# Performance work log

Hardware: AMD Instinct MI355X
Metric: run time of the kernel (lower is better)

Reference implementation:

```python
import jax, jax.numpy as jnp
import numpy as np

N_HEAD = 32
N_KV_HEAD = 8
HD = 64  # head dim
N_EMBD = 2048
B, T = 2, 2048
ROPE_THETA = 10000.0


def _apply_rope(x, cos, sin):
    # x: [B, T, H, HD]; cos/sin: [T, HD//2]. Interleaved complex pairs (even, odd),
    # matching torch.view_as_complex on x.reshape(..., -1, 2).
    x0 = x[..., 0::2]
    x1 = x[..., 1::2]
    c = cos[None, :, None, :]
    s = sin[None, :, None, :]
    o0 = x0 * c - x1 * s
    o1 = x0 * s + x1 * c
    return jnp.stack([o0, o1], axis=-1).reshape(x.shape)


def setup_inputs() -> dict:
    key = jax.random.key(0)
    k1, k2, k3 = jax.random.split(key, 3)
    x = jax.random.normal(k1, (B, T, N_EMBD), dtype=jnp.float32)
    Wqkv = jax.random.normal(k2, ((N_HEAD + 2 * N_KV_HEAD) * HD, N_EMBD), dtype=jnp.float32) * 0.02
    Wproj = jax.random.normal(k3, (N_EMBD, N_EMBD), dtype=jnp.float32) * 0.02
    # precompute_freqs_cis as in llm.c (llama path)
    freqs = 1.0 / (ROPE_THETA ** (np.arange(0, HD, 2, dtype=np.float32) / HD))
    ang = np.outer(np.arange(T, dtype=np.float32), freqs)  # [T, HD//2]
    freqs_cos = jnp.asarray(np.cos(ang), dtype=jnp.float32)
    freqs_sin = jnp.asarray(np.sin(ang), dtype=jnp.float32)
    return {"x": x, "Wqkv": Wqkv, "Wproj": Wproj,
            "freqs_cos": freqs_cos, "freqs_sin": freqs_sin, "start_pos": -1}


def reference(x, Wqkv, Wproj, freqs_cos, freqs_sin, start_pos):
    Bx, Tx, C = x.shape
    n_rep = N_HEAD // N_KV_HEAD
    qkv = x @ Wqkv.T  # [B, T, (H + 2*KV)*HD]
    q = qkv[..., : N_HEAD * HD].reshape(Bx, Tx, N_HEAD, HD)
    k = qkv[..., N_HEAD * HD: (N_HEAD + N_KV_HEAD) * HD].reshape(Bx, Tx, N_KV_HEAD, HD)
    v = qkv[..., (N_HEAD + N_KV_HEAD) * HD:].reshape(Bx, Tx, N_KV_HEAD, HD)
    # RoPE on q, k
    q = _apply_rope(q, freqs_cos, freqs_sin)
    k = _apply_rope(k, freqs_cos, freqs_sin)
    # start_pos < 0: training path, no KV cache. GQA repeat of kv heads.
    k = jnp.repeat(k, n_rep, axis=2)  # [B, T, H, HD]
    v = jnp.repeat(v, n_rep, axis=2)
    q = q.transpose(0, 2, 1, 3)  # [B, H, T, HD]
    k = k.transpose(0, 2, 1, 3)
    v = v.transpose(0, 2, 1, 3)
    scale = 1.0 / np.sqrt(HD).astype(np.float32)
    scores = jnp.einsum("bhtd,bhsd->bhts", q, k) * scale  # [B, H, T, T]
    causal = jnp.tril(jnp.ones((Tx, Tx), dtype=bool))
    scores = jnp.where(causal[None, None, :, :], scores, -jnp.inf)
    att = jax.nn.softmax(scores.astype(jnp.float32), axis=-1).astype(q.dtype)
    y = jnp.einsum("bhts,bhsd->bhtd", att, v)
    y = y.transpose(0, 2, 1, 3).reshape(Bx, Tx, C)
    return y @ Wproj.T
```

## Files before the change

### kernel.cpp

```cpp
#include <hip/hip_runtime.h>
#include <hip/hip_bf16.h>
#include <cstdint>

#define NH   32
#define NKV  8
#define HD   64
#define CE   2048
#define BB   2
#define TT   2048
#define QKVD 3072
#define MM   (BB*TT)

typedef float  f32x4  __attribute__((ext_vector_type(4)));
typedef float  f32x16 __attribute__((ext_vector_type(16)));
typedef short  s16x8  __attribute__((ext_vector_type(8)));
typedef unsigned short u16;

#define AS1 __attribute__((address_space(1)))
#define AS3 __attribute__((address_space(3)))
#define GLDS16(src, dst) __builtin_amdgcn_global_load_lds( \
    (const AS1 uint32_t*)(src), (AS3 uint32_t*)(dst), 16, 0, 0)

static __device__ __forceinline__ float bf2f(u16 u) {
    union { uint32_t u; float f; } v; v.u = ((uint32_t)u) << 16; return v.f;
}
static __device__ __forceinline__ u16 f2bf(float f) {
    union { float f; uint32_t u; } v; v.f = f;
    uint32_t r = v.u + 0x7fffu + ((v.u >> 16) & 1u);
    return (u16)(r >> 16);
}
static __device__ __forceinline__ uint32_t cvtpk(float lo, float hi) {
    uint32_t r;
    asm("v_cvt_pk_bf16_f32 %0, %1, %2" : "=v"(r) : "v"(lo), "v"(hi));
    return r;
}
static __device__ __forceinline__ void plswap(uint32_t &a, uint32_t &b) {
    asm volatile("v_permlane32_swap_b32 %0, %1" : "+v"(a), "+v"(b));
}

static __device__ __forceinline__ void cvt8(const float* __restrict__ in, uint32_t* __restrict__ out) {
    const float4* p = reinterpret_cast<const float4*>(in);
    float4 a = p[0], b = p[1];
    uint4 o;
    o.x = cvtpk(a.x, a.y); o.y = cvtpk(a.z, a.w);
    o.z = cvtpk(b.x, b.y); o.w = cvtpk(b.z, b.w);
    *reinterpret_cast<uint4*>(out) = o;
}
__global__ void k_cvt_all(const float* __restrict__ x, const float* __restrict__ wqkv,
                          const float* __restrict__ wproj,
                          uint32_t* __restrict__ xo, uint32_t* __restrict__ wqo,
                          uint32_t* __restrict__ wpo,
                          const float* __restrict__ fcos, const float* __restrict__ fsin,
                          float2* __restrict__ csT) {
    const int n1 = MM * CE / 8, n2 = QKVD * CE / 8, n3 = CE * CE / 8, n4 = 32 * TT / 8;
    int i = blockIdx.x * blockDim.x + threadIdx.x;
    if (i < n1) {
        cvt8(x + (size_t)i * 8, xo + (size_t)i * 4);
    } else if (i < n1 + n2) {
        int k = i - n1;
        cvt8(wqkv + (size_t)k * 8, wqo + (size_t)k * 4);
    } else if (i < n1 + n2 + n3) {
        int k = i - n1 - n2;
        cvt8(wproj + (size_t)k * 8, wpo + (size_t)k * 4);
    } else if (i < n1 + n2 + n3 + n4) {
        int k = (i - n1 - n2 - n3) * 8;
        #pragma unroll
        for (int jj = 0; jj < 8; ++jj) {
            float2 cs; cs.x = fcos[k + jj]; cs.y = fsin[k + jj];
            csT[k + jj] = cs;
        }
    }
}

__global__ __launch_bounds__(256) void k_gemm_qkv(const u16* __restrict__ A,
                                                  const u16* __restrict__ Bm,
                                                  u16* __restrict__ Qb,
                                                  u16* __restrict__ Kb,
                                                  u16* __restrict__ Vt,
                                                  const float2* __restrict__ csT) {
    __shared__ u16 As[128 * 32];
    __shared__ u16 Bs[128 * 32];
    const int K = CE;
    const int c  = blockIdx.x + 24 * blockIdx.y;
    const int nc = (c & 7) * 96 + (c >> 3);
    const int m0 = (nc / 24) * 128;
    const int n0 = (nc % 24) * 128;

    const int tid  = threadIdx.x;
    const int w    = tid >> 6;
    const int lane = tid & 63;
    const int lr   = lane & 15, lg = lane >> 4;
    const int wm   = (w >> 1) * 64, wn = (w & 1) * 64;

    const int o0 = w * 2048 + lane * 16, o1 = o0 + 1024;
    const int ar0 = o0 >> 6, ar1 = o1 >> 6;
    const int ac0 = (o0 & 63) >> 1, ac1 = (o1 & 63) >> 1;
    const size_t aof0 = (size_t)(m0 + ar0) * K + ac0;
    const size_t aof1 = (size_t)(m0 + ar1) * K + ac1;
    const size_t bof0 = (size_t)(n0 + ar0) * K + ac0;
    const size_t bof1 = (size_t)(n0 + ar1) * K + ac1;
    u16* dA0 = &As[w * 1024];       u16* dA1 = &As[w * 1024 + 512];
    u16* dB0 = &Bs[w * 1024];       u16* dB1 = &Bs[w * 1024 + 512];

    f32x4 acc[4][4] = {};

    for (int k0 = 0; k0 < K; k0 += 32) {
        GLDS16(A  + aof0 + k0, dA0);
        GLDS16(A  + aof1 + k0, dA1);
        GLDS16(Bm + bof0 + k0, dB0);
        GLDS16(Bm + bof1 + k0, dB1);
        __syncthreads();
        s16x8 af[4], bf[4];
        #pragma unroll
        for (int i = 0; i < 4; ++i)
            af[i] = *reinterpret_cast<const s16x8*>(&As[(wm + i * 16 + lr) * 32 + lg * 8]);
        #pragma unroll
        for (int j = 0; j < 4; ++j)
            bf[j] = *reinterpret_cast<const s16x8*>(&Bs[(wn + j * 16 + lr) * 32 + lg * 8]);
        #pragma unroll
        for (int i = 0; i < 4; ++i)
            #pragma unroll
            for (int j = 0; j < 4; ++j)
                acc[i][j] = __builtin_amdgcn_mfma_f32_16x16x32_bf16(af[i], bf[j], acc[i][j], 0, 0, 0);
        __syncthreads();
    }

    const float QS = 0.18033688011112042f;
    const int bb = m0 / TT;
    const int tb = m0 - bb * TT + wm;
    #pragma unroll
    for (int i = 0; i < 4; ++i) {
        const int t0 = tb + i * 16 + lg * 4;
        #pragma unroll
        for (int j = 0; j < 4; ++j) {
            const int n = n0 + wn + j * 16 + lr;
            if (n0 < NH * HD) {
                const int hh = n >> 6, d = n & 63;
                #pragma unroll
                for (int r = 0; r < 4; ++r) {
                    const int t = t0 + r;
                    const float2 cs = csT[t * 32 + (d >> 1)];
                    float v = acc[i][j][r];
                    float p = __shfl_xor(v, 1, 64);
                    float o = ((lr & 1) ? (p * cs.y + v * cs.x) : (v * cs.x - p * cs.y)) * QS;
                    float po = __shfl_xor(o, 1, 64);
                    if (!(lr & 1))
                        *reinterpret_cast<uint32_t*>(Qb + ((size_t)((bb * NH + hh) * TT + t)) * HD + d) = cvtpk(o, po);
                }
            } else if (n0 < (NH + NKV) * HD) {
                const int fk = n - NH * HD;
                const int hh = fk >> 6, d = fk & 63;
                #pragma unroll
                for (int r = 0; r < 4; ++r) {
                    const int t = t0 + r;
                    const float2 cs = csT[t * 32 + (d >> 1)];
                    float v = acc[i][j][r];
                    float p = __shfl_xor(v, 1, 64);
                    float o = (lr & 1) ? (p * cs.y + v * cs.x) : (v * cs.x - p * cs.y);
                    float po = __shfl_xor(o, 1, 64);
                    if (!(lr & 1))
                        *reinterpret_cast<uint32_t*>(Kb + ((size_t)((bb * NKV + hh) * TT + t)) * HD + d) = cvtpk(o, po);
                }
            } else {
                const int fv = n - (NH + NKV) * HD;
                const int vh = fv >> 6, d = fv & 63;
                uint2 st;
                st.x = cvtpk(acc[i][j][0], acc[i][j][1]);
                st.y = cvtpk(acc[i][j][2], acc[i][j][3]);
                *reinterpret_cast<uint2*>(Vt + ((size_t)(bb * NKV + vh) * HD + d) * TT + t0) = st;
            }
        }
    }
}

__global__ __launch_bounds__(256) void k_gemm_bt(const u16* __restrict__ A,
                                                 const u16* __restrict__ Bm,
                                                 float* __restrict__ Cout,
                                                 int M, int N, int K) {
    __shared__ u16 As[128 * 32];
    __shared__ u16 Bs[128 * 32];
    const int c  = blockIdx.x + 16 * blockIdx.y;
    const int nc = (c & 7) * 64 + (c >> 3);
    const int m0 = (nc >> 4) * 128;
    const int n0 = (nc & 15) * 128;

    const int tid  = threadIdx.x;
    const int w    = tid >> 6;
    const int lane = tid & 63;
    const int lr   = lane & 15, lg = lane >> 4;
    const int wm   = (w >> 1) * 64, wn = (w & 1) * 64;

    const int o0 = w * 2048 + lane * 16, o1 = o0 + 1024;
    const int ar0 = o0 >> 6, ar1 = o1 >> 6;
    const int ac0 = (o0 & 63) >> 1, ac1 = (o1 & 63) >> 1;
    const size_t aof0 = (size_t)(m0 + ar0) * K + ac0;
    const size_t aof1 = (size_t)(m0 + ar1) * K + ac1;
    const size_t bof0 = (size_t)(n0 + ar0) * K + ac0;
    const size_t bof1 = (size_t)(n0 + ar1) * K + ac1;
    u16* dA0 = &As[w * 1024];       u16* dA1 = &As[w * 1024 + 512];
    u16* dB0 = &Bs[w * 1024];       u16* dB1 = &Bs[w * 1024 + 512];

    f32x4 acc[4][4] = {};

    for (int k0 = 0; k0 < K; k0 += 32) {
        GLDS16(A  + aof0 + k0, dA0);
        GLDS16(A  + aof1 + k0, dA1);
        GLDS16(Bm + bof0 + k0, dB0);
        GLDS16(Bm + bof1 + k0, dB1);
        __syncthreads();
        s16x8 af[4], bf[4];
        #pragma unroll
        for (int i = 0; i < 4; ++i)
            af[i] = *reinterpret_cast<const s16x8*>(&As[(wm + i * 16 + lr) * 32 + lg * 8]);
        #pragma unroll
        for (int j = 0; j < 4; ++j)
            bf[j] = *reinterpret_cast<const s16x8*>(&Bs[(wn + j * 16 + lr) * 32 + lg * 8]);
        #pragma unroll
        for (int i = 0; i < 4; ++i)
            #pragma unroll
            for (int j = 0; j < 4; ++j)
                acc[i][j] = __builtin_amdgcn_mfma_f32_16x16x32_bf16(af[i], bf[j], acc[i][j], 0, 0, 0);
        __syncthreads();
    }

    #pragma unroll
    for (int i = 0; i < 4; ++i)
        #pragma unroll
        for (int j = 0; j < 4; ++j)
            #pragma unroll
            for (int r = 0; r < 4; ++r) {
                int m = m0 + wm + i * 16 + lg * 4 + r;
                int n = n0 + wn + j * 16 + lr;
                __builtin_nontemporal_store(acc[i][j][r], &Cout[(size_t)m * N + n]);
            }
}

__global__ __launch_bounds__(512) void k_attn(const u16* __restrict__ Q,
                                              const u16* __restrict__ Kb,
                                              const u16* __restrict__ Vt,
                                              u16* __restrict__ Y) {
    __shared__ u16 Ks[2][4096];
    __shared__ u16 Vs[2][4096];

    const int tid = threadIdx.x;
    const int w = tid >> 6, lane = tid & 63;
    const int wv = w & 3, half = w >> 2;
    const int ql = lane & 31, hi = lane >> 5;
    const int hi16 = hi << 4;
    const int b = blockIdx.z, h = blockIdx.y, kvh = h >> 2;
    const int u = blockIdx.x;

    const int m  = b ? (7 - u) : u;
    const int j1 = 2 * m + 1, j2 = 2 * m;
    const int jq = half ? j2 : j1;
    const int q0w  = jq * 128 + wv * 32;
    const int nt   = 2 * j1 + 2;
    const int tmxw = (q0w + 31) >> 6;
    const int qabs = q0w + ql;

    const u16* qbase = Q  + ((size_t)(b * NH  + h  ) * TT) * HD;
    const u16* kbase = Kb + ((size_t)(b * NKV + kvh) * TT) * HD;
    const u16* vbase = Vt + ((size_t)(b * NKV + kvh) * HD) * TT;

    const int o0 = w * 1024 + lane * 16;
    const int r0 = o0 >> 7;
    const int c0 = (o0 & 127) ^ ((r0 & 7) << 4);
    const size_t kof0 = (size_t)r0 * HD + (c0 >> 1);
    const size_t vof0 = (size_t)r0 * TT + (c0 >> 1);

    const char* KsB = (const char*)&Ks[0][0];
    const char* VsB = (const char*)&Vs[0][0];
    const int krb0 = (0 * 32 + ql) * 128, ksz0 = ((0 * 32 + ql) & 7) << 4;
    const int krb1 = (1 * 32 + ql) * 128, ksz1 = ((1 * 32 + ql) & 7) << 4;

    s16x8 qf[4];
    #pragma unroll
    for (int ds = 0; ds < 4; ++ds)
        qf[ds] = *reinterpret_cast<const s16x8*>(qbase + (size_t)qabs * HD + ds * 16 + 8 * hi);
    asm volatile("s_waitcnt vmcnt(0)" ::: "memory");

    GLDS16(kbase + kof0, &Ks[0][w * 512]);
    GLDS16(vbase + vof0, &Vs[0][w * 512]);

    float mrow = -1e30f, lrowp = 0.f;
    f32x16 oT0 = {}, oT1 = {};

    for (int t = 0; t < nt; ++t) {
        const int cur = t & 1;
        const int kv0 = t * 64;
        if (t + 1 < nt) {
            GLDS16(kbase + (size_t)(kv0 + 64) * HD + kof0, &Ks[cur ^ 1][w * 512]);
            GLDS16(vbase + (kv0 + 64) + vof0, &Vs[cur ^ 1][w * 512]);
            asm volatile("s_waitcnt vmcnt(2)" ::: "memory");
        } else {
            asm volatile("s_waitcnt vmcnt(0)" ::: "memory");
        }
        __builtin_amdgcn_s_barrier();
        __builtin_amdgcn_sched_barrier(0);

        if (t <= tmxw) {
            const int bufo = cur * 8192;

            f32x16 sc0 = {}, sc1 = {};
            __builtin_amdgcn_s_setprio(1);
            #pragma unroll
            for (int ds = 0; ds < 4; ++ds) {
                s16x8 k0 = *reinterpret_cast<const s16x8*>(KsB + bufo + krb0 + (((ds << 5) | hi16) ^ ksz0));
                s16x8 k1 = *reinterpret_cast<const s16x8*>(KsB + bufo + krb1 + (((ds << 5) | hi16) ^ ksz1));
                sc0 = __builtin_amdgcn_mfma_f32_32x32x16_bf16(k0, qf[ds], sc0, 0, 0, 0);
                sc1 = __builtin_amdgcn_mfma_f32_32x32x16_bf16(k1, qf[ds], sc1, 0, 0, 0);
            }
            __builtin_amdgcn_s_setprio(0);

            float p0[16], p1[16];
            #pragma unroll
            for (int r = 0; r < 16; ++r) { p0[r] = sc0[r]; p1[r] = sc1[r]; }

            if (t == tmxw) {
                const int dq = qabs - kv0 - 4 * hi;
                #pragma unroll
                for (int r = 0; r < 16; ++r) {
                    const int kr = (r & 3) + 8 * (r >> 2);
                    p0[r] = (kr      <= dq) ? p0[r] : -1e30f;
                    p1[r] = (kr + 32 <= dq) ? p1[r] : -1e30f;
                }
            }

            float tmax = fmaxf(p0[0], p1[0]);
            #pragma unroll
            for (int r = 1; r < 16; ++r) tmax = fmaxf(fmaxf(tmax, p0[r]), p1[r]);
            if (__any(tmax > mrow + 8.f)) {
                float tf = fmaxf(tmax, __shfl_xor(tmax, 32, 64));
                float mn = fmaxf(mrow, tf);
                float alpha = __builtin_amdgcn_exp2f(mrow - mn);
                mrow = mn;
                lrowp *= alpha;
                #pragma unroll
                for (int r = 0; r < 16; ++r) { oT0[r] *= alpha; oT1[r] *= alpha; }
            }

            float sum = 0.f;
            #pragma unroll
            for (int r = 0; r < 16; ++r) {
                p0[r] = __builtin_amdgcn_exp2f(p0[r] - mrow);
                p1[r] = __builtin_amdgcn_exp2f(p1[r] - mrow);
                sum += p0[r] + p1[r];
            }
            lrowp += sum;

            __builtin_amdgcn_s_setprio(1);
            #pragma unroll
            for (int ks = 0; ks < 2; ++ks) {
                uint32_t a0 = cvtpk(p0[ks * 8 + 0], p0[ks * 8 + 1]);
                uint32_t b0 = cvtpk(p0[ks * 8 + 4], p0[ks * 8 + 5]);
                plswap(a0, b0);
                uint32_t a1 = cvtpk(p0[ks * 8 + 2], p0[ks * 8 + 3]);
                uint32_t b1 = cvtpk(p0[ks * 8 + 6], p0[ks * 8 + 7]);
                plswap(a1, b1);
                union { uint32_t d[4]; s16x8 v; } pb;
                pb.d[0] = a0; pb.d[1] = a1; pb.d[2] = b0; pb.d[3] = b1;
                const int colb = (0 << 6) | (ks << 5) | hi16;
                s16x8 v0 = *reinterpret_cast<const s16x8*>(VsB + bufo + krb0 + (colb ^ ksz0));
                s16x8 v1 = *reinterpret_cast<const s16x8*>(VsB + bufo + krb1 + (colb ^ ksz1));
                oT0 = __builtin_amdgcn_mfma_f32_32x32x16_bf16(v0, pb.v, oT0, 0, 0, 0);
                oT1 = __builtin_amdgcn_mfma_f32_32x32x16_bf16(v1, pb.v, oT1, 0, 0, 0);
            }
            #pragma unroll
            for (int ks = 0; ks < 2; ++ks) {
                uint32_t a0 = cvtpk(p1[ks * 8 + 0], p1[ks * 8 + 1]);
                uint32_t b0 = cvtpk(p1[ks * 8 + 4], p1[ks * 8 + 5]);
                plswap(a0, b0);
                uint32_t a1 = cvtpk(p1[ks * 8 + 2], p1[ks * 8 + 3]);
                uint32_t b1 = cvtpk(p1[ks * 8 + 6], p1[ks * 8 + 7]);
                plswap(a1, b1);
                union { uint32_t d[4]; s16x8 v; } pb;
                pb.d[0] = a0; pb.d[1] = a1; pb.d[2] = b0; pb.d[3] = b1;
                const int colb = (1 << 6) | (ks << 5) | hi16;
                s16x8 v0 = *reinterpret_cast<const s16x8*>(VsB + bufo + krb0 + (colb ^ ksz0));
                s16x8 v1 = *reinterpret_cast<const s16x8*>(VsB + bufo + krb1 + (colb ^ ksz1));
                oT0 = __builtin_amdgcn_mfma_f32_32x32x16_bf16(v0, pb.v, oT0, 0, 0, 0);
                oT1 = __builtin_amdgcn_mfma_f32_32x32x16_bf16(v1, pb.v, oT1, 0, 0, 0);
            }
            __builtin_amdgcn_s_setprio(0);
        }

        __builtin_amdgcn_sched_barrier(0);
        __builtin_amdgcn_s_barrier();
    }

    lrowp += __shfl_xor(lrowp, 32, 64);
    const float rinv = 1.f / lrowp;
    const size_t yrow = ((size_t)(b * TT + qabs) * NH + h) * HD;
    #pragma unroll
    for (int rp = 0; rp < 8; ++rp) {
        const int d = ((2 * rp) & 3) + 8 * (rp >> 1) + 4 * hi;
        *reinterpret_cast<uint32_t*>(Y + yrow + d) =
            cvtpk(oT0[2 * rp] * rinv, oT0[2 * rp + 1] * rinv);
        *reinterpret_cast<uint32_t*>(Y + yrow + 32 + d) =
            cvtpk(oT1[2 * rp] * rinv, oT1[2 * rp + 1] * rinv);
    }
}

extern "C" void kernel_launch(void* const* d_in, const int* in_sizes, int n_in,
                              void* d_out, int out_size, void* d_ws, size_t ws_size,
                              hipStream_t stream) {
    (void)in_sizes; (void)n_in; (void)out_size; (void)ws_size;
    const float* x     = (const float*)d_in[0];
    const float* wqkv  = (const float*)d_in[1];
    const float* wproj = (const float*)d_in[2];
    const float* fcos  = (const float*)d_in[3];
    const float* fsin  = (const float*)d_in[4];

    char* ws = (char*)d_ws;
    size_t off = 0;
    auto alloc = [&](size_t bytes) { void* p = ws + off; off += (bytes + 255) & ~(size_t)255; return p; };
    u16*    Xbf  = (u16*)alloc((size_t)MM * CE * 2);
    u16*    Wqb  = (u16*)alloc((size_t)QKVD * CE * 2);
    u16*    Wpb  = (u16*)alloc((size_t)CE * CE * 2);
    u16*    Qb   = (u16*)alloc((size_t)BB * NH * TT * HD * 2);
    u16*    Kbuf = (u16*)alloc((size_t)BB * NKV * TT * HD * 2);
    u16*    Vtb  = (u16*)alloc((size_t)BB * NKV * HD * TT * 2);
    u16*    Yb   = (u16*)alloc((size_t)MM * CE * 2);
    float2* csT  = (float2*)alloc((size_t)32 * TT * sizeof(float2));

    const int ncvt = MM * CE / 8 + QKVD * CE / 8 + CE * CE / 8 + 32 * TT / 8;
    k_cvt_all<<<(ncvt + 255) / 256, 256, 0, stream>>>(x, wqkv, wproj,
                                                      (uint32_t*)Xbf, (uint32_t*)Wqb, (uint32_t*)Wpb,
                                                      fcos, fsin, csT);

    dim3 g1(QKVD / 128, MM / 128);
    k_gemm_qkv<<<g1, 256, 0, stream>>>(Xbf, Wqb, Qb, Kbuf, Vtb, csT);

    dim3 ga(8, NH, BB);
    k_attn<<<ga, 512, 0, stream>>>(Qb, Kbuf, Vtb, Yb);

    dim3 g2(CE / 128, MM / 128);
    k_gemm_bt<<<g2, 256, 0, stream>>>(Yb, Wpb, (float*)d_out, MM, CE, CE);
}
```

Measured before the change: 207.9 us.

## Double GEMM K-tile to 64 with XOR-swizzled LDS and batched RoPE epilogue

Both bf16 GEMM kernels now stage a 64-wide K slice per iteration instead of 32. That halves the number of barrier pairs and global-to-LDS rounds, and doubles the MFMA work between syncs. The LDS layout uses a row-based XOR swizzle on the global source column so fragment reads avoid bank conflicts. The QKV epilogue merges the Q and K RoPE paths and packs values to bf16 before the pair shuffle, which cuts the number of shuffles. The RoPE inputs are therefore rounded to bf16 before rotation, a small precision change, and LDS use per block doubles.

```diff
diff --git a/kernel.cpp b/kernel.cpp
--- a/kernel.cpp
+++ b/kernel.cpp
@@ -78,8 +78,8 @@
                                                   u16* __restrict__ Kb,
                                                   u16* __restrict__ Vt,
                                                   const float2* __restrict__ csT) {
-    __shared__ u16 As[128 * 32];
-    __shared__ u16 Bs[128 * 32];
+    __shared__ u16 As[128 * 64];
+    __shared__ u16 Bs[128 * 64];
     const int K = CE;
     const int c  = blockIdx.x + 24 * blockIdx.y;
     const int nc = (c & 7) * 96 + (c >> 3);
@@ -92,76 +92,104 @@
     const int lr   = lane & 15, lg = lane >> 4;
     const int wm   = (w >> 1) * 64, wn = (w & 1) * 64;
 
-    const int o0 = w * 2048 + lane * 16, o1 = o0 + 1024;
-    const int ar0 = o0 >> 6, ar1 = o1 >> 6;
-    const int ac0 = (o0 & 63) >> 1, ac1 = (o1 & 63) >> 1;
-    const size_t aof0 = (size_t)(m0 + ar0) * K + ac0;
-    const size_t aof1 = (size_t)(m0 + ar1) * K + ac1;
-    const size_t bof0 = (size_t)(n0 + ar0) * K + ac0;
-    const size_t bof1 = (size_t)(n0 + ar1) * K + ac1;
-    u16* dA0 = &As[w * 1024];       u16* dA1 = &As[w * 1024 + 512];
-    u16* dB0 = &Bs[w * 1024];       u16* dB1 = &Bs[w * 1024 + 512];
+    const int rr = tid >> 3;
+    const int cc = (tid & 7) * 16;
+    const int csw = cc ^ ((rr & 7) << 4);
+    size_t aof[4], bof[4];
+    #pragma unroll
+    for (int s = 0; s < 4; ++s) {
+        const int r = s * 32 + rr;
+        aof[s] = (size_t)(m0 + r) * K + (csw >> 1);
+        bof[s] = (size_t)(n0 + r) * K + (csw >> 1);
+    }
 
     f32x4 acc[4][4] = {};
 
-    for (int k0 = 0; k0 < K; k0 += 32) {
-        GLDS16(A  + aof0 + k0, dA0);
-        GLDS16(A  + aof1 + k0, dA1);
-        GLDS16(Bm + bof0 + k0, dB0);
-        GLDS16(Bm + bof1 + k0, dB1);
+    for (int k0 = 0; k0 < K; k0 += 64) {
+        #pragma unroll
+        for (int s = 0; s < 4; ++s)
+            GLDS16(A + aof[s] + k0, (u16*)((char*)As + s * 4096 + tid * 16));
+        #pragma unroll
+        for (int s = 0; s < 4; ++s)
+            GLDS16(Bm + bof[s] + k0, (u16*)((char*)Bs + s * 4096 + tid * 16));
         __syncthreads();
-        s16x8 af[4], bf[4];
-        #pragma unroll
-        for (int i = 0; i < 4; ++i)
-            af[i] = *reinterpret_cast<const s16x8*>(&As[(wm + i * 16 + lr) * 32 + lg * 8]);
-        #pragma unroll
-        for (int j = 0; j < 4; ++j)
-            bf[j] = *reinterpret_cast<const s16x8*>(&Bs[(wn + j * 16 + lr) * 32 + lg * 8]);
-        #pragma unroll
-        for (int i = 0; i < 4; ++i)
-            #pragma unroll
-            for (int j = 0; j < 4; ++j)
-                acc[i][j] = __builtin_amdgcn_mfma_f32_16x16x32_bf16(af[i], bf[j], acc[i][j], 0, 0, 0);
+        s16x8 af[4][2], bf[4][2];
+        #pragma unroll
+        for (int i = 0; i < 4; ++i) {
+            const int ra = wm + i * 16 + lr;
+            const int x = (ra & 7) << 4;
+            af[i][0] = *reinterpret_cast<const s16x8*>((const char*)As + ra * 128 + ((lg * 16) ^ x));
+            af[i][1] = *reinterpret_cast<const s16x8*>((const char*)As + ra * 128 + ((64 + lg * 16) ^ x));
+        }
+        #pragma unroll
+        for (int j = 0; j < 4; ++j) {
+            const int rb = wn + j * 16 + lr;
+            const int x = (rb & 7) << 4;
+            bf[j][0] = *reinterpret_cast<const s16x8*>((const char*)Bs + rb * 128 + ((lg * 16) ^ x));
+            bf[j][1] = *reinterpret_cast<const s16x8*>((const char*)Bs + rb * 128 + ((64 + lg * 16) ^ x));
+        }
+        #pragma unroll
+        for (int kk = 0; kk < 2; ++kk)
+            #pragma unroll
+            for (int i = 0; i < 4; ++i)
+                #pragma unroll
+                for (int j = 0; j < 4; ++j)
+                    acc[i][j] = __builtin_amdgcn_mfma_f32_16x16x32_bf16(af[i][kk], bf[j][kk], acc[i][j], 0, 0, 0);
         __syncthreads();
     }
 
     const float QS = 0.18033688011112042f;
     const int bb = m0 / TT;
     const int tb = m0 - bb * TT + wm;
-    #pragma unroll
-    for (int i = 0; i < 4; ++i) {
-        const int t0 = tb + i * 16 + lg * 4;
-        #pragma unroll
-        for (int j = 0; j < 4; ++j) {
-            const int n = n0 + wn + j * 16 + lr;
-            if (n0 < NH * HD) {
-                const int hh = n >> 6, d = n & 63;
+    if (n0 < (NH + NKV) * HD) {
+        const bool isq = (n0 < NH * HD);
+        const bool odd = lr & 1;
+        #pragma unroll
+        for (int i = 0; i < 4; ++i) {
+            const int t0 = tb + i * 16 + lg * 4;
+            #pragma unroll
+            for (int j = 0; j < 4; ++j) {
+                const int n = n0 + wn + j * 16 + lr;
+                const int d = n & 63;
+                uint32_t m01 = cvtpk(acc[i][j][0], acc[i][j][1]);
+                uint32_t m23 = cvtpk(acc[i][j][2], acc[i][j][3]);
+                uint32_t p01 = __shfl_xor(m01, 1, 64);
+                uint32_t p23 = __shfl_xor(m23, 1, 64);
+                float o_[4];
                 #pragma unroll
                 for (int r = 0; r < 4; ++r) {
-                    const int t = t0 + r;
-                    const float2 cs = csT[t * 32 + (d >> 1)];
-                    float v = acc[i][j][r];
-                    float p = __shfl_xor(v, 1, 64);
-                    float o = ((lr & 1) ? (p * cs.y + v * cs.x) : (v * cs.x - p * cs.y)) * QS;
-                    float po = __shfl_xor(o, 1, 64);
-                    if (!(lr & 1))
-                        *reinterpret_cast<uint32_t*>(Qb + ((size_t)((bb * NH + hh) * TT + t)) * HD + d) = cvtpk(o, po);
+                    uint32_t mo = (r < 2) ? m01 : m23;
+                    uint32_t po = (r < 2) ? p01 : p23;
+                    u16 own = (r & 1) ? (u16)(mo >> 16) : (u16)(mo & 0xffff);
+                    u16 par = (r & 1) ? (u16)(po >> 16) : (u16)(po & 0xffff);
+                    float x0 = bf2f(odd ? par : own);
+                    float x1 = bf2f(odd ? own : par);
+                    const float2 cs2 = csT[(t0 + r) * 32 + (d >> 1)];
+                    float o = odd ? (x0 * cs2.y + x1 * cs2.x) : (x0 * cs2.x - x1 * cs2.y);
+                    o_[r] = isq ? o * QS : o;
                 }
-            } else if (n0 < (NH + NKV) * HD) {
-                const int fk = n - NH * HD;
-                const int hh = fk >> 6, d = fk & 63;
-                #pragma unroll
-                for (int r = 0; r < 4; ++r) {
-                    const int t = t0 + r;
-                    const float2 cs = csT[t * 32 + (d >> 1)];
-                    float v = acc[i][j][r];
-                    float p = __shfl_xor(v, 1, 64);
-                    float o = (lr & 1) ? (p * cs.y + v * cs.x) : (v * cs.x - p * cs.y);
-                    float po = __shfl_xor(o, 1, 64);
-                    if (!(lr & 1))
-                        *reinterpret_cast<uint32_t*>(Kb + ((size_t)((bb * NKV + hh) * TT + t)) * HD + d) = cvtpk(o, po);
+                uint32_t o01 = cvtpk(o_[0], o_[1]);
+                uint32_t o23 = cvtpk(o_[2], o_[3]);
+                uint32_t q01 = __shfl_xor(o01, 1, 64);
+                uint32_t q23 = __shfl_xor(o23, 1, 64);
+                if (!odd) {
+                    const int hh = isq ? (n >> 6) : ((n - NH * HD) >> 6);
+                    u16* base = isq ? (Qb + ((size_t)(bb * NH + hh) * TT + t0) * HD + d)
+                                    : (Kb + ((size_t)(bb * NKV + hh) * TT + t0) * HD + d);
+                    *reinterpret_cast<uint32_t*>(base + 0 * HD) = (o01 & 0xffffu) | (q01 << 16);
+                    *reinterpret_cast<uint32_t*>(base + 1 * HD) = (o01 >> 16) | (q01 & 0xffff0000u);
+                    *reinterpret_cast<uint32_t*>(base + 2 * HD) = (o23 & 0xffffu) | (q23 << 16);
+                    *reinterpret_cast<uint32_t*>(base + 3 * HD) = (o23 >> 16) | (q23 & 0xffff0000u);
                 }
-            } else {
+            }
+        }
+    } else {
+        #pragma unroll
+        for (int i = 0; i < 4; ++i) {
+            const int t0 = tb + i * 16 + lg * 4;
+            #pragma unroll
+            for (int j = 0; j < 4; ++j) {
+                const int n = n0 + wn + j * 16 + lr;
                 const int fv = n - (NH + NKV) * HD;
                 const int vh = fv >> 6, d = fv & 63;
                 uint2 st;
@@ -177,8 +205,8 @@
                                                  const u16* __restrict__ Bm,
                                                  float* __restrict__ Cout,
                                                  int M, int N, int K) {
-    __shared__ u16 As[128 * 32];
-    __shared__ u16 Bs[128 * 32];
+    __shared__ u16 As[128 * 64];
+    __shared__ u16 Bs[128 * 64];
     const int c  = blockIdx.x + 16 * blockIdx.y;
     const int nc = (c & 7) * 64 + (c >> 3);
     const int m0 = (nc >> 4) * 128;
@@ -190,36 +218,49 @@
     const int lr   = lane & 15, lg = lane >> 4;
     const int wm   = (w >> 1) * 64, wn = (w & 1) * 64;
 
-    const int o0 = w * 2048 + lane * 16, o1 = o0 + 1024;
-    const int ar0 = o0 >> 6, ar1 = o1 >> 6;
-    const int ac0 = (o0 & 63) >> 1, ac1 = (o1 & 63) >> 1;
-    const size_t aof0 = (size_t)(m0 + ar0) * K + ac0;
-    const size_t aof1 = (size_t)(m0 + ar1) * K + ac1;
-    const size_t bof0 = (size_t)(n0 + ar0) * K + ac0;
-    const size_t bof1 = (size_t)(n0 + ar1) * K + ac1;
-    u16* dA0 = &As[w * 1024];       u16* dA1 = &As[w * 1024 + 512];
-    u16* dB0 = &Bs[w * 1024];       u16* dB1 = &Bs[w * 1024 + 512];
+    const int rr = tid >> 3;
+    const int cc = (tid & 7) * 16;
+    const int csw = cc ^ ((rr & 7) << 4);
+    size_t aof[4], bof[4];
+    #pragma unroll
+    for (int s = 0; s < 4; ++s) {
+        const int r = s * 32 + rr;
+        aof[s] = (size_t)(m0 + r) * K + (csw >> 1);
+        bof[s] = (size_t)(n0 + r) * K + (csw >> 1);
+    }
 
     f32x4 acc[4][4] = {};
 
-    for (int k0 = 0; k0 < K; k0 += 32) {
-        GLDS16(A  + aof0 + k0, dA0);
-        GLDS16(A  + aof1 + k0, dA1);
-        GLDS16(Bm + bof0 + k0, dB0);
-        GLDS16(Bm + bof1 + k0, dB1);
+    for (int k0 = 0; k0 < K; k0 += 64) {
+        #pragma unroll
+        for (int s = 0; s < 4; ++s)
+            GLDS16(A + aof[s] + k0, (u16*)((char*)As + s * 4096 + tid * 16));
+        #pragma unroll
+        for (int s = 0; s < 4; ++s)
+            GLDS16(Bm + bof[s] + k0, (u16*)((char*)Bs + s * 4096 + tid * 16));
         __syncthreads();
-        s16x8 af[4], bf[4];
-        #pragma unroll
-        for (int i = 0; i < 4; ++i)
-            af[i] = *reinterpret_cast<const s16x8*>(&As[(wm + i * 16 + lr) * 32 + lg * 8]);
-        #pragma unroll
-        for (int j = 0; j < 4; ++j)
-            bf[j] = *reinterpret_cast<const s16x8*>(&Bs[(wn + j * 16 + lr) * 32 + lg * 8]);
-        #pragma unroll
-        for (int i = 0; i < 4; ++i)
-            #pragma unroll
-            for (int j = 0; j < 4; ++j)
-                acc[i][j] = __builtin_amdgcn_mfma_f32_16x16x32_bf16(af[i], bf[j], acc[i][j], 0, 0, 0);
+        s16x8 af[4][2], bf[4][2];
+        #pragma unroll
+        for (int i = 0; i < 4; ++i) {
+            const int ra = wm + i * 16 + lr;
+            const int x = (ra & 7) << 4;
+            af[i][0] = *reinterpret_cast<const s16x8*>((const char*)As + ra * 128 + ((lg * 16) ^ x));
+            af[i][1] = *reinterpret_cast<const s16x8*>((const char*)As + ra * 128 + ((64 + lg * 16) ^ x));
+        }
+        #pragma unroll
+        for (int j = 0; j < 4; ++j) {
+            const int rb = wn + j * 16 + lr;
+            const int x = (rb & 7) << 4;
+            bf[j][0] = *reinterpret_cast<const s16x8*>((const char*)Bs + rb * 128 + ((lg * 16) ^ x));
+            bf[j][1] = *reinterpret_cast<const s16x8*>((const char*)Bs + rb * 128 + ((64 + lg * 16) ^ x));
+        }
+        #pragma unroll
+        for (int kk = 0; kk < 2; ++kk)
+            #pragma unroll
+            for (int i = 0; i < 4; ++i)
+                #pragma unroll
+                for (int j = 0; j < 4; ++j)
+                    acc[i][j] = __builtin_amdgcn_mfma_f32_16x16x32_bf16(af[i][kk], bf[j][kk], acc[i][j], 0, 0, 0);
         __syncthreads();
     }
 
```

New measurement: 213.1 us. +2.5%, slower.
